# Kernel tuning notes

Hardware: AMD Instinct MI355X
Metric: run time of the kernel (lower is better)

## Reference

```python
import jax, jax.numpy as jnp
import numpy as np

N_NODES = 50000
N_EDGES = 640000
D = 128
L = 3


def setup_inputs() -> dict:
    key = jax.random.key(0)
    k1, k2, k3, k4 = jax.random.split(key, 4)
    x = jax.random.normal(k1, (N_NODES, D), dtype=jnp.float32)
    # Glorot-ish scale so activations stay O(1) across 3 layers
    Ws = jax.random.normal(k2, (L, D, D), dtype=jnp.float32) * (1.0 / np.sqrt(D))
    bs = jnp.zeros((L, D), dtype=jnp.float32)
    edge_src = jax.random.randint(k3, (N_EDGES,), 0, N_NODES, dtype=jnp.int32)
    edge_dst = jax.random.randint(k4, (N_EDGES,), 0, N_NODES, dtype=jnp.int32)
    return {"x": x, "Ws": Ws, "bs": bs, "edge_src": edge_src, "edge_dst": edge_dst}


def reference(x, Ws, bs, edge_src, edge_dst):
    n = x.shape[0]
    ones = jnp.ones(edge_src.shape[0], dtype=x.dtype)
    # degrees, clamped to 1 as in dgl GraphConv(norm='both')
    deg_out = jnp.maximum(jax.ops.segment_sum(ones, edge_src, num_segments=n), 1.0)
    deg_in = jnp.maximum(jax.ops.segment_sum(ones, edge_dst, num_segments=n), 1.0)
    inv_sqrt_out = jax.lax.rsqrt(deg_out)[:, None]  # [N,1]
    inv_sqrt_in = jax.lax.rsqrt(deg_in)[:, None]    # [N,1]
    for l in range(Ws.shape[0]):
        h = x * inv_sqrt_out                         # src normalization
        msg = h[edge_src]                            # [E,D] gather
        agg = jax.ops.segment_sum(msg, edge_dst, num_segments=n)  # [N,D] scatter-add
        h = agg * inv_sqrt_in                        # dst normalization
        x = jax.nn.relu(h @ Ws[l] + bs[l])           # linear + ReLU
    return x
```

## Files before the change

### kernel.cpp

```cpp
#include <hip/hip_runtime.h>
#include <hip/hip_fp16.h>

typedef __attribute__((ext_vector_type(8))) _Float16 half8;
typedef __attribute__((ext_vector_type(4))) float f32x4;
typedef unsigned int u32;
typedef unsigned short u16;
typedef unsigned long long u64;

#define ELL_PAD 64
#define BKT 128
#define BKT_SH 7
#define EPB 2048
#define NAMAX 512
#define RUNCAP 3072


__global__ __launch_bounds__(256) void initpack(int* __restrict__ deg_out,
                                                u32* __restrict__ xz0,
                                                u32* __restrict__ xz1,
                                                const float* __restrict__ Ws,
                                                _Float16* __restrict__ Whi,
                                                _Float16* __restrict__ Wlo,
                                                int N, int padU32, int zb, int packTotal) {
  int b = blockIdx.x;
  if (b < zb) {
    int i = b * 256 + threadIdx.x;
    if (i < N) deg_out[i] = 0;
    if (b == 0) {
      for (int j = threadIdx.x; j < padU32; j += 256) { xz0[j] = 0; xz1[j] = 0; }
    }
    return;
  }
  int i = (b - zb) * 256 + threadIdx.x;
  if (i < packTotal) {
    int lane  = i & 63;
    int kstep = (i >> 6) & 3;
    int ntile = (i >> 8) & 7;
    int layer = i >> 11;
    int nn = ntile * 16 + (lane & 15);
    int k0 = kstep * 32 + (lane >> 4) * 8;
    const float* W = Ws + (size_t)layer * 128 * 128;
    size_t base = (size_t)i * 8;
    for (int j = 0; j < 8; j++) {
      float v = W[(k0 + j) * 128 + nn];
      _Float16 hi = (_Float16)v;
      Whi[base + j] = hi;
      Wlo[base + j] = (_Float16)(v - (float)hi);
    }
  }
}


__global__ __launch_bounds__(512) void parta(const int* __restrict__ esrc,
                                             const int* __restrict__ edst,
                                             int* __restrict__ deg_out,
                                             u32* __restrict__ part,
                                             u32* __restrict__ runTab,
                                             int E, int NB) {
  __shared__ u32 hist[512];
  __shared__ u32 stage[EPB];
  __shared__ u32 scanA[512];
  int a = blockIdx.x;
  int e0 = a * EPB;
  int e1 = min(E, e0 + EPB);
  int len = e1 - e0;
  int tid = threadIdx.x;
  if (tid <= NB) hist[tid] = 0;
  __syncthreads();
  for (int i = e0 + tid; i < e1; i += 512) {
    int s = esrc[i];
    int d = edst[i];
    atomicAdd(&deg_out[s], 1);
    atomicAdd(&hist[d >> BKT_SH], 1u);
  }
  __syncthreads();
  u32 myc = (tid < NB) ? hist[tid] : 0;
  scanA[tid] = myc;
  __syncthreads();
  for (int off = 1; off < NB; off <<= 1) {
    u32 t = scanA[tid] + ((tid >= off) ? scanA[tid - off] : 0);
    __syncthreads();
    scanA[tid] = t;
    __syncthreads();
  }
  u32 excl = scanA[tid] - myc;
  u32* rt = runTab + (size_t)a * (NB + 1);
  if (tid < NB) { rt[tid] = excl; hist[tid] = excl; }
  if (tid == 0) rt[NB] = (u32)len;
  __syncthreads();
  for (int i = e0 + tid; i < e1; i += 512) {
    int s = esrc[i];
    int d = edst[i];
    u32 p = atomicAdd(&hist[d >> BKT_SH], 1u);
    stage[p] = (u32)s | ((u32)(d & (BKT - 1)) << 16);
  }
  __syncthreads();
  u32* op = part + (size_t)a * EPB;
  for (int j = tid; j < len; j += 512) op[j] = stage[j];
}


__global__ __launch_bounds__(512) void partb(const u32* __restrict__ part,
                                             const u32* __restrict__ runTab,
                                             int* __restrict__ deg_in,
                                             u16* __restrict__ ell,
                                             int N, int NA, int NB) {
  __shared__ u16 slice[BKT * ELL_PAD];
  __shared__ u32 cnt2[BKT * 17];
  __shared__ u32 roff[NAMAX + 1];
  __shared__ u32 rbase[NAMAX];
  __shared__ u16 runid[RUNCAP];
  __shared__ u32 pstage[RUNCAP];
  __shared__ u32 scanA[512];
  int b = blockIdx.x;
  int base = b * BKT;
  int hi = min(BKT, N - base);
  if (hi <= 0) return;
  int tid = threadIdx.x;

  u32 nv = ((u32)N << 16) | (u32)N;
  u32* s32 = (u32*)slice;
  for (int j = tid; j < BKT * (ELL_PAD / 2); j += 512) s32[j] = nv;
  for (int j = tid; j < BKT * 17; j += 512) cnt2[j] = 0;
  u32 mylen = 0;
  if (tid < NA) {
    u32 s = runTab[(size_t)tid * (NB + 1) + b];
    u32 e = runTab[(size_t)tid * (NB + 1) + b + 1];
    mylen = e - s;
    rbase[tid] = (u32)tid * EPB + s;
  }
  scanA[tid] = mylen;
  __syncthreads();
  for (int off = 1; off < NA + 1; off <<= 1) {
    u32 t = scanA[tid] + ((tid >= off) ? scanA[tid - off] : 0);
    __syncthreads();
    scanA[tid] = t;
    __syncthreads();
  }
  if (tid <= NA) roff[tid] = scanA[tid] - mylen;
  __syncthreads();
  int T = (int)roff[NA];
  for (int a = tid; a < NA; a += 512) {
    u32 s0 = roff[a];
    u32 l  = roff[a + 1] - s0;
    for (u32 k = 0; k < l; k++)
      if (s0 + k < RUNCAP) runid[s0 + k] = (u16)a;
  }
  __syncthreads();
  for (int i = tid; i < T; i += 512) {
    int a;
    if (i < RUNCAP) a = runid[i];
    else {
      int lo = 0, hh = NA;
      while (hh - lo > 1) { int mid = (lo + hh) >> 1; if (roff[mid] <= (u32)i) lo = mid; else hh = mid; }
      a = lo;
    }
    u32 pair = part[(size_t)rbase[a] + ((u32)i - roff[a])];
    if (i < RUNCAP) pstage[i] = pair;
    u32 dl  = pair >> 16;
    u32 src = pair & 0xFFFFu;
    atomicAdd(&cnt2[dl * 17 + (src >> 12)], 1u);
  }
  __syncthreads();
  if (tid < BKT) {
    u32 run = 0;
    for (int bk = 0; bk < 16; bk++) {
      u32 t = cnt2[tid * 17 + bk];
      cnt2[tid * 17 + bk] = run;
      run += t;
    }
    if (tid < hi) deg_in[base + tid] = (int)run;
  }
  __syncthreads();
  for (int i = tid; i < T; i += 512) {
    u32 pair;
    if (i < RUNCAP) pair = pstage[i];
    else {
      int lo = 0, hh = NA;
      while (hh - lo > 1) { int mid = (lo + hh) >> 1; if (roff[mid] <= (u32)i) lo = mid; else hh = mid; }
      pair = part[(size_t)rbase[lo] + ((u32)i - roff[lo])];
    }
    u32 dl  = pair >> 16;
    u32 src = pair & 0xFFFFu;
    u32 p = atomicAdd(&cnt2[dl * 17 + (src >> 12)], 1u);
    if (p < ELL_PAD) slice[dl * ELL_PAD + p] = (u16)src;
  }
  __syncthreads();
  u32* eg = (u32*)(ell + (size_t)base * ELL_PAD);
  for (int j = tid; j < hi * (ELL_PAD / 2); j += 512) eg[j] = s32[j];
}


__global__ __launch_bounds__(256) void xscale(const float* __restrict__ x,
                                              const int* __restrict__ deg_out,
                                              __half2* __restrict__ xh, int n64) {
  int gid = blockIdx.x * 256 + threadIdx.x;
  if (gid >= n64) return;
  int row = gid >> 6;
  int d = deg_out[row]; if (d < 1) d = 1;
  float s = rsqrtf((float)d);
  float2 v = ((const float2*)x)[gid];
  xh[gid] = __floats2half2_rn(v.x * s, v.y * s);
}


__global__ __launch_bounds__(512) void layer16(const _Float16* __restrict__ xh,
                                               const int* __restrict__ deg_in,
                                               const u16* __restrict__ ell,
                                               const _Float16* __restrict__ Whi,
                                               const _Float16* __restrict__ Wlo,
                                               const float* __restrict__ bias,
                                               const int* __restrict__ deg_out,
                                               __half* __restrict__ out16,
                                               float* __restrict__ out32, int n) {
  __shared__ _Float16 As[16 * 136];
  const int wave = threadIdx.x >> 6;
  const int lane = threadIdx.x & 63;
  const int sub  = lane & 15;
  const int grp  = lane >> 4;
  const int sh   = grp << 4;
  const u32 sub16 = (u32)sub * 16u;
  const int rowBase = blockIdx.x * 16;
  const char* __restrict__ xb = (const char*)xh;

  {
    int r0 = rowBase + wave * 2, r1 = r0 + 1;
    int d0 = (r0 < n) ? deg_in[r0] : 0;
    int d1 = (r1 < n) ? deg_in[r1] : 0;
    int l0 = d0 > ELL_PAD ? ELL_PAD : d0;
    int l1 = d1 > ELL_PAD ? ELL_PAD : d1;
    int t0 = (l0 + 3) & ~3;
    int t1 = (l1 + 3) & ~3;
    const u16* ep0 = ell + (u32)(r0 < n ? r0 : 0) * ELL_PAD;
    const u16* ep1 = ell + (u32)(r1 < n ? r1 : 0) * ELL_PAD;

    float a0[8] = {0.f, 0.f, 0.f, 0.f, 0.f, 0.f, 0.f, 0.f};
    float a1[8] = {0.f, 0.f, 0.f, 0.f, 0.f, 0.f, 0.f, 0.f};

    int m = t0 < t1 ? t0 : t1;
    int e = 0;
    for (; e + 8 <= m; e += 8) {
      u64 wa0 = *(const u64*)&ep0[e];
      u64 wa1 = *(const u64*)&ep0[e + 4];
      u64 wb0 = *(const u64*)&ep1[e];
      u64 wb1 = *(const u64*)&ep1[e + 4];
      u32 ia0 = ((u32)(wa0 >> sh) & 0xFFFFu) * 256u + sub16;
      u32 ia1 = ((u32)(wa1 >> sh) & 0xFFFFu) * 256u + sub16;
      u32 ib0 = ((u32)(wb0 >> sh) & 0xFFFFu) * 256u + sub16;
      u32 ib1 = ((u32)(wb1 >> sh) & 0xFFFFu) * 256u + sub16;
      half8 va0 = *(const half8*)(xb + ia0);
      half8 va1 = *(const half8*)(xb + ia1);
      half8 vb0 = *(const half8*)(xb + ib0);
      half8 vb1 = *(const half8*)(xb + ib1);
#pragma unroll
      for (int j = 0; j < 8; j++) {
        a0[j] += (float)va0[j] + (float)va1[j];
        a1[j] += (float)vb0[j] + (float)vb1[j];
      }
    }
    for (; e < m; e += 4) {
      u64 wa = *(const u64*)&ep0[e];
      u64 wb = *(const u64*)&ep1[e];
      u32 ia = ((u32)(wa >> sh) & 0xFFFFu) * 256u + sub16;
      u32 ib = ((u32)(wb >> sh) & 0xFFFFu) * 256u + sub16;
      half8 va = *(const half8*)(xb + ia);
      half8 vb = *(const half8*)(xb + ib);
#pragma unroll
      for (int j = 0; j < 8; j++) { a0[j] += (float)va[j]; a1[j] += (float)vb[j]; }
    }
    for (int ea = m; ea < t0; ea += 4) {
      u64 wa = *(const u64*)&ep0[ea];
      u32 ia = ((u32)(wa >> sh) & 0xFFFFu) * 256u + sub16;
      half8 va = *(const half8*)(xb + ia);
#pragma unroll
      for (int j = 0; j < 8; j++) a0[j] += (float)va[j];
    }
    for (int eb = m; eb < t1; eb += 4) {
      u64 wb = *(const u64*)&ep1[eb];
      u32 ib = ((u32)(wb >> sh) & 0xFFFFu) * 256u + sub16;
      half8 vb = *(const half8*)(xb + ib);
#pragma unroll
      for (int j = 0; j < 8; j++) a1[j] += (float)vb[j];
    }

#pragma unroll
    for (int j = 0; j < 8; j++) {
      a0[j] += __shfl_xor(a0[j], 16, 64);
      a0[j] += __shfl_xor(a0[j], 32, 64);
      a1[j] += __shfl_xor(a1[j], 16, 64);
      a1[j] += __shfl_xor(a1[j], 32, 64);
    }

    float si0 = rsqrtf((float)(d0 < 1 ? 1 : d0));
    float si1 = rsqrtf((float)(d1 < 1 ? 1 : d1));
    if (grp == 0) {
      half8 h0, h1;
#pragma unroll
      for (int j = 0; j < 8; j++) {
        h0[j] = (_Float16)(a0[j] * si0);
        h1[j] = (_Float16)(a1[j] * si1);
      }
      *(half8*)&As[(wave * 2 + 0) * 136 + sub * 8] = h0;
      *(half8*)&As[(wave * 2 + 1) * 136 + sub * 8] = h1;
    }
  }
  __syncthreads();

  f32x4 acc = (f32x4){0.f, 0.f, 0.f, 0.f};
#pragma unroll
  for (int ks = 0; ks < 4; ks++) {
    half8 a  = *(const half8*)&As[(size_t)sub * 136 + ks * 32 + grp * 8];
    half8 bh = *(const half8*)&Whi[((wave * 4 + ks) * 64 + lane) * 8];
    half8 bl = *(const half8*)&Wlo[((wave * 4 + ks) * 64 + lane) * 8];
    acc = __builtin_amdgcn_mfma_f32_16x16x32_f16(a, bh, acc, 0, 0, 0);
    acc = __builtin_amdgcn_mfma_f32_16x16x32_f16(a, bl, acc, 0, 0, 0);
  }

  const int r0c = rowBase + grp * 4;
  const int col = wave * 16 + sub;
  const float bv = bias[col];
#pragma unroll
  for (int r = 0; r < 4; r++) {
    int row = r0c + r;
    if (row < n) {
      float v = fmaxf(acc[r] + bv, 0.f);
      if (out16) {
        int d = deg_out[row]; if (d < 1) d = 1;
        out16[(size_t)row * 128 + col] = __float2half(v * rsqrtf((float)d));
      } else {
        out32[(size_t)row * 128 + col] = v;
      }
    }
  }
}


extern "C" void kernel_launch(void* const* d_in, const int* in_sizes, int n_in,
                              void* d_out, int out_size, void* d_ws, size_t ws_size,
                              hipStream_t stream) {
  const float* x   = (const float*)d_in[0];
  const float* Ws  = (const float*)d_in[1];
  const float* bs  = (const float*)d_in[2];
  const int* esrc  = (const int*)d_in[3];
  const int* edst  = (const int*)d_in[4];

  const int D = 128;
  const int N = in_sizes[0] / D;
  const int E = in_sizes[3];
  const int L = in_sizes[1] / (D * D);
  const int Npad = ((N + 15) / 16) * 16;
  const int NA = (E + EPB - 1) / EPB;
  const int NB = (N + BKT - 1) / BKT;

  char* base = (char*)d_ws;
  size_t off = 0;
  auto alloc = [&](size_t bytes) {
    char* p = base + off;
    off = (off + bytes + 255) & ~(size_t)255;
    return p;
  };
  int*      deg_out = (int*)alloc((size_t)N * 4);
  int*      deg_in  = (int*)alloc((size_t)N * 4);
  u16*      ell     = (u16*)alloc((size_t)N * ELL_PAD * 2);
  _Float16* Whi     = (_Float16*)alloc((size_t)L * 16384 * 2);
  _Float16* Wlo     = (_Float16*)alloc((size_t)L * 16384 * 2);
  _Float16* xh0     = (_Float16*)alloc((size_t)(Npad + 16) * 128 * 2);
  _Float16* xh1     = (_Float16*)alloc((size_t)(Npad + 16) * 128 * 2);
  u32*      part    = (u32*)alloc((size_t)NA * EPB * 4);
  u32*      runTab  = (u32*)alloc((size_t)NA * (NB + 1) * 4);

  const int zb = (N + 255) / 256;
  const int packTotal = L * 2048;
  const int packB = (packTotal + 255) / 256;
  const int padU32 = 16 * 64;

  initpack<<<dim3(zb + packB), dim3(256), 0, stream>>>(
      deg_out,
      (u32*)(xh0 + (size_t)N * 128), (u32*)(xh1 + (size_t)N * 128),
      Ws, Whi, Wlo, N, padU32, zb, packTotal);
  parta<<<dim3(NA), dim3(512), 0, stream>>>(
      esrc, edst, deg_out, part, runTab, E, NB);
  partb<<<dim3(NB), dim3(512), 0, stream>>>(
      part, runTab, deg_in, ell, N, NA, NB);
  xscale<<<dim3((N * 64 + 255) / 256), dim3(256), 0, stream>>>(
      x, deg_out, (__half2*)xh0, N * 64);

  float* outf = (float*)d_out;
  _Float16* ping[2] = {xh0, xh1};
  const dim3 lgrid(Npad / 16), lblk(512);

  for (int l = 0; l < L; l++) {
    bool last = (l == L - 1);
    layer16<<<lgrid, lblk, 0, stream>>>(
        (const _Float16*)ping[l & 1], deg_in, ell,
        Whi + (size_t)l * 16384, Wlo + (size_t)l * 16384,
        bs + (size_t)l * D, deg_out,
        last ? nullptr : (__half*)ping[(l + 1) & 1],
        last ? outf : nullptr, N);
  }
}
```

Baseline: 241.6 us.

## Fuse all stages into one persistent cooperative kernel with grid syncs

Replaces the sequence of separate kernels (init/pack, two-pass edge partitioning, x scaling, three layer kernels) with a single persistent cooperative kernel. Stages are separated by grid-wide barriers, and blocks loop over work items. The x scaling step is folded into the ELL-build stage, and one union shared-memory buffer is reused across phases. This targets launch overhead and inter-kernel gaps. The costs are that grid size is capped by occupancy, which may lower parallelism in the heavy gather stage, and the large shared-memory footprint may limit blocks per CU.

New measurement: 485.3 us. 2.01x slower.

```diff
diff --git a/kernel.cpp b/kernel.cpp
--- a/kernel.cpp
+++ b/kernel.cpp
@@ -1,5 +1,8 @@
 #include <hip/hip_runtime.h>
 #include <hip/hip_fp16.h>
+#include <hip/hip_cooperative_groups.h>
+
+namespace cg = cooperative_groups;
 
 typedef __attribute__((ext_vector_type(8))) _Float16 half8;
 typedef __attribute__((ext_vector_type(4))) float f32x4;
@@ -15,320 +18,308 @@
 #define RUNCAP 3072
 
 
-__global__ __launch_bounds__(256) void initpack(int* __restrict__ deg_out,
-                                                u32* __restrict__ xz0,
-                                                u32* __restrict__ xz1,
-                                                const float* __restrict__ Ws,
-                                                _Float16* __restrict__ Whi,
-                                                _Float16* __restrict__ Wlo,
-                                                int N, int padU32, int zb, int packTotal) {
-  int b = blockIdx.x;
-  if (b < zb) {
-    int i = b * 256 + threadIdx.x;
-    if (i < N) deg_out[i] = 0;
-    if (b == 0) {
-      for (int j = threadIdx.x; j < padU32; j += 256) { xz0[j] = 0; xz1[j] = 0; }
+struct Par {
+  const float* x; const float* Ws; const float* bs;
+  const int* esrc; const int* edst;
+  int* deg_out; int* deg_in;
+  u16* ell; _Float16* Whi; _Float16* Wlo;
+  _Float16* xh0; _Float16* xh1; float* outf;
+  u32* part; u32* runTab;
+  int N, E, L, NA, NB, tiles, packTotal, padU32;
+};
+
+__global__ __launch_bounds__(512) void fused_all(Par p) {
+  __shared__ __align__(16) char smem[49680];
+  cg::grid_group grid = cg::this_grid();
+  const int tid = threadIdx.x;
+
+  {
+    int gt = blockIdx.x * 512 + tid, gs = gridDim.x * 512;
+    for (int i = gt; i < p.N; i += gs) p.deg_out[i] = 0;
+    u32* xz0 = (u32*)(p.xh0 + (size_t)p.N * 128);
+    u32* xz1 = (u32*)(p.xh1 + (size_t)p.N * 128);
+    for (int j = gt; j < p.padU32; j += gs) { xz0[j] = 0; xz1[j] = 0; }
+    for (int i = gt; i < p.packTotal; i += gs) {
+      int lane = i & 63, kstep = (i >> 6) & 3, ntile = (i >> 8) & 7, layer = i >> 11;
+      int nn = ntile * 16 + (lane & 15);
+      int k0 = kstep * 32 + (lane >> 4) * 8;
+      const float* W = p.Ws + (size_t)layer * 128 * 128;
+      size_t base = (size_t)i * 8;
+      for (int j = 0; j < 8; j++) {
+        float v = W[(k0 + j) * 128 + nn];
+        _Float16 hi = (_Float16)v;
+        p.Whi[base + j] = hi;
+        p.Wlo[base + j] = (_Float16)(v - (float)hi);
+      }
     }
-    return;
-  }
-  int i = (b - zb) * 256 + threadIdx.x;
-  if (i < packTotal) {
-    int lane  = i & 63;
-    int kstep = (i >> 6) & 3;
-    int ntile = (i >> 8) & 7;
-    int layer = i >> 11;
-    int nn = ntile * 16 + (lane & 15);
-    int k0 = kstep * 32 + (lane >> 4) * 8;
-    const float* W = Ws + (size_t)layer * 128 * 128;
-    size_t base = (size_t)i * 8;
-    for (int j = 0; j < 8; j++) {
-      float v = W[(k0 + j) * 128 + nn];
-      _Float16 hi = (_Float16)v;
-      Whi[base + j] = hi;
-      Wlo[base + j] = (_Float16)(v - (float)hi);
+  }
+  grid.sync();
+
+  {
+    u32* hist  = (u32*)smem;
+    u32* stage = (u32*)(smem + 2048);
+    u32* scanA = (u32*)(smem + 10240);
+    for (int a = blockIdx.x; a < p.NA; a += gridDim.x) {
+      __syncthreads();
+      int e0 = a * EPB, e1 = min(p.E, e0 + EPB), len = e1 - e0;
+      if (tid <= p.NB) hist[tid] = 0;
+      __syncthreads();
+      for (int i = e0 + tid; i < e1; i += 512) {
+        int s = p.esrc[i], d = p.edst[i];
+        atomicAdd(&p.deg_out[s], 1);
+        atomicAdd(&hist[d >> BKT_SH], 1u);
+      }
+      __syncthreads();
+      u32 myc = (tid < p.NB) ? hist[tid] : 0;
+      scanA[tid] = myc;
+      __syncthreads();
+      for (int off = 1; off < p.NB; off <<= 1) {
+        u32 t2 = scanA[tid] + ((tid >= off) ? scanA[tid - off] : 0);
+        __syncthreads();
+        scanA[tid] = t2;
+        __syncthreads();
+      }
+      u32 excl = scanA[tid] - myc;
+      u32* rt = p.runTab + (size_t)a * (p.NB + 1);
+      if (tid < p.NB) { rt[tid] = excl; hist[tid] = excl; }
+      if (tid == 0) rt[p.NB] = (u32)len;
+      __syncthreads();
+      for (int i = e0 + tid; i < e1; i += 512) {
+        int s = p.esrc[i], d = p.edst[i];
+        u32 q = atomicAdd(&hist[d >> BKT_SH], 1u);
+        stage[q] = (u32)s | ((u32)(d & (BKT - 1)) << 16);
+      }
+      __syncthreads();
+      u32* op = p.part + (size_t)a * EPB;
+      for (int j = tid; j < len; j += 512) op[j] = stage[j];
     }
   }
-}
-
-
-__global__ __launch_bounds__(512) void parta(const int* __restrict__ esrc,
-                                             const int* __restrict__ edst,
-                                             int* __restrict__ deg_out,
-                                             u32* __restrict__ part,
-                                             u32* __restrict__ runTab,
-                                             int E, int NB) {
-  __shared__ u32 hist[512];
-  __shared__ u32 stage[EPB];
-  __shared__ u32 scanA[512];
-  int a = blockIdx.x;
-  int e0 = a * EPB;
-  int e1 = min(E, e0 + EPB);
-  int len = e1 - e0;
-  int tid = threadIdx.x;
-  if (tid <= NB) hist[tid] = 0;
-  __syncthreads();
-  for (int i = e0 + tid; i < e1; i += 512) {
-    int s = esrc[i];
-    int d = edst[i];
-    atomicAdd(&deg_out[s], 1);
-    atomicAdd(&hist[d >> BKT_SH], 1u);
-  }
-  __syncthreads();
-  u32 myc = (tid < NB) ? hist[tid] : 0;
-  scanA[tid] = myc;
-  __syncthreads();
-  for (int off = 1; off < NB; off <<= 1) {
-    u32 t = scanA[tid] + ((tid >= off) ? scanA[tid - off] : 0);
-    __syncthreads();
-    scanA[tid] = t;
-    __syncthreads();
-  }
-  u32 excl = scanA[tid] - myc;
-  u32* rt = runTab + (size_t)a * (NB + 1);
-  if (tid < NB) { rt[tid] = excl; hist[tid] = excl; }
-  if (tid == 0) rt[NB] = (u32)len;
-  __syncthreads();
-  for (int i = e0 + tid; i < e1; i += 512) {
-    int s = esrc[i];
-    int d = edst[i];
-    u32 p = atomicAdd(&hist[d >> BKT_SH], 1u);
-    stage[p] = (u32)s | ((u32)(d & (BKT - 1)) << 16);
-  }
-  __syncthreads();
-  u32* op = part + (size_t)a * EPB;
-  for (int j = tid; j < len; j += 512) op[j] = stage[j];
-}
-
-
-__global__ __launch_bounds__(512) void partb(const u32* __restrict__ part,
-                                             const u32* __restrict__ runTab,
-                                             int* __restrict__ deg_in,
-                                             u16* __restrict__ ell,
-                                             int N, int NA, int NB) {
-  __shared__ u16 slice[BKT * ELL_PAD];
-  __shared__ u32 cnt2[BKT * 17];
-  __shared__ u32 roff[NAMAX + 1];
-  __shared__ u32 rbase[NAMAX];
-  __shared__ u16 runid[RUNCAP];
-  __shared__ u32 pstage[RUNCAP];
-  __shared__ u32 scanA[512];
-  int b = blockIdx.x;
-  int base = b * BKT;
-  int hi = min(BKT, N - base);
-  if (hi <= 0) return;
-  int tid = threadIdx.x;
-
-  u32 nv = ((u32)N << 16) | (u32)N;
-  u32* s32 = (u32*)slice;
-  for (int j = tid; j < BKT * (ELL_PAD / 2); j += 512) s32[j] = nv;
-  for (int j = tid; j < BKT * 17; j += 512) cnt2[j] = 0;
-  u32 mylen = 0;
-  if (tid < NA) {
-    u32 s = runTab[(size_t)tid * (NB + 1) + b];
-    u32 e = runTab[(size_t)tid * (NB + 1) + b + 1];
-    mylen = e - s;
-    rbase[tid] = (u32)tid * EPB + s;
-  }
-  scanA[tid] = mylen;
-  __syncthreads();
-  for (int off = 1; off < NA + 1; off <<= 1) {
-    u32 t = scanA[tid] + ((tid >= off) ? scanA[tid - off] : 0);
-    __syncthreads();
-    scanA[tid] = t;
-    __syncthreads();
-  }
-  if (tid <= NA) roff[tid] = scanA[tid] - mylen;
-  __syncthreads();
-  int T = (int)roff[NA];
-  for (int a = tid; a < NA; a += 512) {
-    u32 s0 = roff[a];
-    u32 l  = roff[a + 1] - s0;
-    for (u32 k = 0; k < l; k++)
-      if (s0 + k < RUNCAP) runid[s0 + k] = (u16)a;
-  }
-  __syncthreads();
-  for (int i = tid; i < T; i += 512) {
-    int a;
-    if (i < RUNCAP) a = runid[i];
-    else {
-      int lo = 0, hh = NA;
-      while (hh - lo > 1) { int mid = (lo + hh) >> 1; if (roff[mid] <= (u32)i) lo = mid; else hh = mid; }
-      a = lo;
+  grid.sync();
+
+  {
+    u16* slice  = (u16*)smem;
+    u32* cnt2   = (u32*)(smem + 16384);
+    u32* roff   = (u32*)(smem + 25088);
+    u32* rbase  = (u32*)(smem + 27140);
+    u16* runid  = (u16*)(smem + 29188);
+    u32* pstage = (u32*)(smem + 35332);
+    u32* scanB  = (u32*)(smem + 47620);
+    for (int b = blockIdx.x; b < p.NB; b += gridDim.x) {
+      __syncthreads();
+      int base = b * BKT;
+      int hi = min(BKT, p.N - base);
+      if (hi <= 0) continue;
+      u32 nv = ((u32)p.N << 16) | (u32)p.N;
+      u32* s32 = (u32*)slice;
+      for (int j = tid; j < BKT * (ELL_PAD / 2); j += 512) s32[j] = nv;
+      for (int j = tid; j < BKT * 17; j += 512) cnt2[j] = 0;
+      u32 mylen = 0;
+      if (tid < p.NA) {
+        u32 s = p.runTab[(size_t)tid * (p.NB + 1) + b];
+        u32 e = p.runTab[(size_t)tid * (p.NB + 1) + b + 1];
+        mylen = e - s;
+        rbase[tid] = (u32)tid * EPB + s;
+      }
+      scanB[tid] = mylen;
+      __syncthreads();
+      for (int off = 1; off < p.NA + 1; off <<= 1) {
+        u32 t2 = scanB[tid] + ((tid >= off) ? scanB[tid - off] : 0);
+        __syncthreads();
+        scanB[tid] = t2;
+        __syncthreads();
+      }
+      if (tid <= p.NA) roff[tid] = scanB[tid] - mylen;
+      __syncthreads();
+      int T = (int)roff[p.NA];
+      for (int a = tid; a < p.NA; a += 512) {
+        u32 s0 = roff[a];
+        u32 l = roff[a + 1] - s0;
+        for (u32 k = 0; k < l; k++)
+          if (s0 + k < RUNCAP) runid[s0 + k] = (u16)a;
+      }
+      __syncthreads();
+      for (int i = tid; i < T; i += 512) {
+        int a;
+        if (i < RUNCAP) a = runid[i];
+        else {
+          int lo = 0, hh = p.NA;
+          while (hh - lo > 1) { int mid = (lo + hh) >> 1; if (roff[mid] <= (u32)i) lo = mid; else hh = mid; }
+          a = lo;
+        }
+        u32 pair = p.part[(size_t)rbase[a] + ((u32)i - roff[a])];
+        if (i < RUNCAP) pstage[i] = pair;
+        u32 dl = pair >> 16;
+        u32 src = pair & 0xFFFFu;
+        atomicAdd(&cnt2[dl * 17 + (src >> 12)], 1u);
+      }
+      __syncthreads();
+      if (tid < BKT) {
+        u32 run = 0;
+        for (int bk = 0; bk < 16; bk++) {
+          u32 t2 = cnt2[tid * 17 + bk];
+          cnt2[tid * 17 + bk] = run;
+          run += t2;
+        }
+        if (tid < hi) p.deg_in[base + tid] = (int)run;
+      }
+      __syncthreads();
+      for (int i = tid; i < T; i += 512) {
+        u32 pair;
+        if (i < RUNCAP) pair = pstage[i];
+        else {
+          int lo = 0, hh = p.NA;
+          while (hh - lo > 1) { int mid = (lo + hh) >> 1; if (roff[mid] <= (u32)i) lo = mid; else hh = mid; }
+          pair = p.part[(size_t)rbase[lo] + ((u32)i - roff[lo])];
+        }
+        u32 dl = pair >> 16;
+        u32 src = pair & 0xFFFFu;
+        u32 q = atomicAdd(&cnt2[dl * 17 + (src >> 12)], 1u);
+        if (q < ELL_PAD) slice[dl * ELL_PAD + q] = (u16)src;
+      }
+      __syncthreads();
+      u32* eg = (u32*)(p.ell + (size_t)base * ELL_PAD);
+      for (int j = tid; j < hi * (ELL_PAD / 2); j += 512) eg[j] = s32[j];
+      float* sc = (float*)scanB;
+      if (tid < hi) {
+        int d = p.deg_out[base + tid]; if (d < 1) d = 1;
+        sc[tid] = rsqrtf((float)d);
+      }
+      __syncthreads();
+      __half2* xh2 = (__half2*)p.xh0;
+      for (int j = tid; j < hi * 64; j += 512) {
+        int r = j >> 6, c = j & 63;
+        float s = sc[r];
+        float2 v = ((const float2*)p.x)[(size_t)(base + r) * 64 + c];
+        xh2[(size_t)(base + r) * 64 + c] = __floats2half2_rn(v.x * s, v.y * s);
+      }
     }
-    u32 pair = part[(size_t)rbase[a] + ((u32)i - roff[a])];
-    if (i < RUNCAP) pstage[i] = pair;
-    u32 dl  = pair >> 16;
-    u32 src = pair & 0xFFFFu;
-    atomicAdd(&cnt2[dl * 17 + (src >> 12)], 1u);
-  }
-  __syncthreads();
-  if (tid < BKT) {
-    u32 run = 0;
-    for (int bk = 0; bk < 16; bk++) {
-      u32 t = cnt2[tid * 17 + bk];
-      cnt2[tid * 17 + bk] = run;
-      run += t;
-    }
-    if (tid < hi) deg_in[base + tid] = (int)run;
-  }
-  __syncthreads();
-  for (int i = tid; i < T; i += 512) {
-    u32 pair;
-    if (i < RUNCAP) pair = pstage[i];
-    else {
-      int lo = 0, hh = NA;
-      while (hh - lo > 1) { int mid = (lo + hh) >> 1; if (roff[mid] <= (u32)i) lo = mid; else hh = mid; }
-      pair = part[(size_t)rbase[lo] + ((u32)i - roff[lo])];
-    }
-    u32 dl  = pair >> 16;
-    u32 src = pair & 0xFFFFu;
-    u32 p = atomicAdd(&cnt2[dl * 17 + (src >> 12)], 1u);
-    if (p < ELL_PAD) slice[dl * ELL_PAD + p] = (u16)src;
-  }
-  __syncthreads();
-  u32* eg = (u32*)(ell + (size_t)base * ELL_PAD);
-  for (int j = tid; j < hi * (ELL_PAD / 2); j += 512) eg[j] = s32[j];
-}
-
-
-__global__ __launch_bounds__(256) void xscale(const float* __restrict__ x,
-                                              const int* __restrict__ deg_out,
-                                              __half2* __restrict__ xh, int n64) {
-  int gid = blockIdx.x * 256 + threadIdx.x;
-  if (gid >= n64) return;
-  int row = gid >> 6;
-  int d = deg_out[row]; if (d < 1) d = 1;
-  float s = rsqrtf((float)d);
-  float2 v = ((const float2*)x)[gid];
-  xh[gid] = __floats2half2_rn(v.x * s, v.y * s);
-}
-
-
-__global__ __launch_bounds__(512) void layer16(const _Float16* __restrict__ xh,
-                                               const int* __restrict__ deg_in,
-                                               const u16* __restrict__ ell,
-                                               const _Float16* __restrict__ Whi,
-                                               const _Float16* __restrict__ Wlo,
-                                               const float* __restrict__ bias,
-                                               const int* __restrict__ deg_out,
-                                               __half* __restrict__ out16,
-                                               float* __restrict__ out32, int n) {
-  __shared__ _Float16 As[16 * 136];
-  const int wave = threadIdx.x >> 6;
-  const int lane = threadIdx.x & 63;
-  const int sub  = lane & 15;
-  const int grp  = lane >> 4;
-  const int sh   = grp << 4;
-  const u32 sub16 = (u32)sub * 16u;
-  const int rowBase = blockIdx.x * 16;
-  const char* __restrict__ xb = (const char*)xh;
-
-  {
-    int r0 = rowBase + wave * 2, r1 = r0 + 1;
-    int d0 = (r0 < n) ? deg_in[r0] : 0;
-    int d1 = (r1 < n) ? deg_in[r1] : 0;
-    int l0 = d0 > ELL_PAD ? ELL_PAD : d0;
-    int l1 = d1 > ELL_PAD ? ELL_PAD : d1;
-    int t0 = (l0 + 3) & ~3;
-    int t1 = (l1 + 3) & ~3;
-    const u16* ep0 = ell + (u32)(r0 < n ? r0 : 0) * ELL_PAD;
-    const u16* ep1 = ell + (u32)(r1 < n ? r1 : 0) * ELL_PAD;
-
-    float a0[8] = {0.f, 0.f, 0.f, 0.f, 0.f, 0.f, 0.f, 0.f};
-    float a1[8] = {0.f, 0.f, 0.f, 0.f, 0.f, 0.f, 0.f, 0.f};
-
-    int m = t0 < t1 ? t0 : t1;
-    int e = 0;
-    for (; e + 8 <= m; e += 8) {
-      u64 wa0 = *(const u64*)&ep0[e];
-      u64 wa1 = *(const u64*)&ep0[e + 4];
-      u64 wb0 = *(const u64*)&ep1[e];
-      u64 wb1 = *(const u64*)&ep1[e + 4];
-      u32 ia0 = ((u32)(wa0 >> sh) & 0xFFFFu) * 256u + sub16;
-      u32 ia1 = ((u32)(wa1 >> sh) & 0xFFFFu) * 256u + sub16;
-      u32 ib0 = ((u32)(wb0 >> sh) & 0xFFFFu) * 256u + sub16;
-      u32 ib1 = ((u32)(wb1 >> sh) & 0xFFFFu) * 256u + sub16;
-      half8 va0 = *(const half8*)(xb + ia0);
-      half8 va1 = *(const half8*)(xb + ia1);
-      half8 vb0 = *(const half8*)(xb + ib0);
-      half8 vb1 = *(const half8*)(xb + ib1);
-#pragma unroll
-      for (int j = 0; j < 8; j++) {
-        a0[j] += (float)va0[j] + (float)va1[j];
-        a1[j] += (float)vb0[j] + (float)vb1[j];
-      }
-    }
-    for (; e < m; e += 4) {
-      u64 wa = *(const u64*)&ep0[e];
-      u64 wb = *(const u64*)&ep1[e];
-      u32 ia = ((u32)(wa >> sh) & 0xFFFFu) * 256u + sub16;
-      u32 ib = ((u32)(wb >> sh) & 0xFFFFu) * 256u + sub16;
-      half8 va = *(const half8*)(xb + ia);
-      half8 vb = *(const half8*)(xb + ib);
-#pragma unroll
-      for (int j = 0; j < 8; j++) { a0[j] += (float)va[j]; a1[j] += (float)vb[j]; }
-    }
-    for (int ea = m; ea < t0; ea += 4) {
-      u64 wa = *(const u64*)&ep0[ea];
-      u32 ia = ((u32)(wa >> sh) & 0xFFFFu) * 256u + sub16;
-      half8 va = *(const half8*)(xb + ia);
-#pragma unroll
-      for (int j = 0; j < 8; j++) a0[j] += (float)va[j];
-    }
-    for (int eb = m; eb < t1; eb += 4) {
-      u64 wb = *(const u64*)&ep1[eb];
-      u32 ib = ((u32)(wb >> sh) & 0xFFFFu) * 256u + sub16;
-      half8 vb = *(const half8*)(xb + ib);
-#pragma unroll
-      for (int j = 0; j < 8; j++) a1[j] += (float)vb[j];
-    }
-
-#pragma unroll
-    for (int j = 0; j < 8; j++) {
-      a0[j] += __shfl_xor(a0[j], 16, 64);
-      a0[j] += __shfl_xor(a0[j], 32, 64);
-      a1[j] += __shfl_xor(a1[j], 16, 64);
-      a1[j] += __shfl_xor(a1[j], 32, 64);
-    }
-
-    float si0 = rsqrtf((float)(d0 < 1 ? 1 : d0));
-    float si1 = rsqrtf((float)(d1 < 1 ? 1 : d1));
-    if (grp == 0) {
-      half8 h0, h1;
-#pragma unroll
-      for (int j = 0; j < 8; j++) {
-        h0[j] = (_Float16)(a0[j] * si0);
-        h1[j] = (_Float16)(a1[j] * si1);
-      }
-      *(half8*)&As[(wave * 2 + 0) * 136 + sub * 8] = h0;
-      *(half8*)&As[(wave * 2 + 1) * 136 + sub * 8] = h1;
-    }
-  }
-  __syncthreads();
-
-  f32x4 acc = (f32x4){0.f, 0.f, 0.f, 0.f};
-#pragma unroll
-  for (int ks = 0; ks < 4; ks++) {
-    half8 a  = *(const half8*)&As[(size_t)sub * 136 + ks * 32 + grp * 8];
-    half8 bh = *(const half8*)&Whi[((wave * 4 + ks) * 64 + lane) * 8];
-    half8 bl = *(const half8*)&Wlo[((wave * 4 + ks) * 64 + lane) * 8];
-    acc = __builtin_amdgcn_mfma_f32_16x16x32_f16(a, bh, acc, 0, 0, 0);
-    acc = __builtin_amdgcn_mfma_f32_16x16x32_f16(a, bl, acc, 0, 0, 0);
-  }
-
-  const int r0c = rowBase + grp * 4;
-  const int col = wave * 16 + sub;
-  const float bv = bias[col];
-#pragma unroll
-  for (int r = 0; r < 4; r++) {
-    int row = r0c + r;
-    if (row < n) {
-      float v = fmaxf(acc[r] + bv, 0.f);
-      if (out16) {
-        int d = deg_out[row]; if (d < 1) d = 1;
-        out16[(size_t)row * 128 + col] = __float2half(v * rsqrtf((float)d));
-      } else {
-        out32[(size_t)row * 128 + col] = v;
+  }
+
+  for (int l = 0; l < p.L; l++) {
+    grid.sync();
+    const _Float16* xin = (l & 1) ? p.xh1 : p.xh0;
+    bool last = (l == p.L - 1);
+    __half* o16 = last ? nullptr : (__half*)((l & 1) ? p.xh0 : p.xh1);
+    float* o32 = last ? p.outf : nullptr;
+    const _Float16* Wh = p.Whi + (size_t)l * 16384;
+    const _Float16* Wl = p.Wlo + (size_t)l * 16384;
+    const float* bias = p.bs + (size_t)l * 128;
+    _Float16* As = (_Float16*)smem;
+    const int wave = tid >> 6, lane = tid & 63, sub = lane & 15, grp = lane >> 4;
+    const int sh = grp << 4;
+    const u32 sub16 = (u32)sub * 16u;
+    const char* xb = (const char*)xin;
+
+    for (int t = blockIdx.x; t < p.tiles; t += gridDim.x) {
+      __syncthreads();
+      int rowBase = t * 16;
+      {
+        int r0 = rowBase + wave * 2, r1 = r0 + 1;
+        int d0 = (r0 < p.N) ? p.deg_in[r0] : 0;
+        int d1 = (r1 < p.N) ? p.deg_in[r1] : 0;
+        int l0 = d0 > ELL_PAD ? ELL_PAD : d0;
+        int l1 = d1 > ELL_PAD ? ELL_PAD : d1;
+        int t0 = (l0 + 3) & ~3;
+        int t1 = (l1 + 3) & ~3;
+        const u16* ep0 = p.ell + (u32)(r0 < p.N ? r0 : 0) * ELL_PAD;
+        const u16* ep1 = p.ell + (u32)(r1 < p.N ? r1 : 0) * ELL_PAD;
+
+        float a0[8] = {0.f, 0.f, 0.f, 0.f, 0.f, 0.f, 0.f, 0.f};
+        float a1[8] = {0.f, 0.f, 0.f, 0.f, 0.f, 0.f, 0.f, 0.f};
+
+        int m = t0 < t1 ? t0 : t1;
+        int e = 0;
+        for (; e + 8 <= m; e += 8) {
+          u64 wa0 = *(const u64*)&ep0[e];
+          u64 wa1 = *(const u64*)&ep0[e + 4];
+          u64 wb0 = *(const u64*)&ep1[e];
+          u64 wb1 = *(const u64*)&ep1[e + 4];
+          u32 ia0 = ((u32)(wa0 >> sh) & 0xFFFFu) * 256u + sub16;
+          u32 ia1 = ((u32)(wa1 >> sh) & 0xFFFFu) * 256u + sub16;
+          u32 ib0 = ((u32)(wb0 >> sh) & 0xFFFFu) * 256u + sub16;
+          u32 ib1 = ((u32)(wb1 >> sh) & 0xFFFFu) * 256u + sub16;
+          half8 va0 = *(const half8*)(xb + ia0);
+          half8 va1 = *(const half8*)(xb + ia1);
+          half8 vb0 = *(const half8*)(xb + ib0);
+          half8 vb1 = *(const half8*)(xb + ib1);
+#pragma unroll
+          for (int j = 0; j < 8; j++) {
+            a0[j] += (float)va0[j] + (float)va1[j];
+            a1[j] += (float)vb0[j] + (float)vb1[j];
+          }
+        }
+        for (; e < m; e += 4) {
+          u64 wa = *(const u64*)&ep0[e];
+          u64 wb = *(const u64*)&ep1[e];
+          u32 ia = ((u32)(wa >> sh) & 0xFFFFu) * 256u + sub16;
+          u32 ib = ((u32)(wb >> sh) & 0xFFFFu) * 256u + sub16;
+          half8 va = *(const half8*)(xb + ia);
+          half8 vb = *(const half8*)(xb + ib);
+#pragma unroll
+          for (int j = 0; j < 8; j++) { a0[j] += (float)va[j]; a1[j] += (float)vb[j]; }
+        }
+        for (int ea = m; ea < t0; ea += 4) {
+          u64 wa = *(const u64*)&ep0[ea];
+          u32 ia = ((u32)(wa >> sh) & 0xFFFFu) * 256u + sub16;
+          half8 va = *(const half8*)(xb + ia);
+#pragma unroll
+          for (int j = 0; j < 8; j++) a0[j] += (float)va[j];
+        }
+        for (int eb = m; eb < t1; eb += 4) {
+          u64 wb = *(const u64*)&ep1[eb];
+          u32 ib = ((u32)(wb >> sh) & 0xFFFFu) * 256u + sub16;
+          half8 vb = *(const half8*)(xb + ib);
+#pragma unroll
+          for (int j = 0; j < 8; j++) a1[j] += (float)vb[j];
+        }
+
+#pragma unroll
+        for (int j = 0; j < 8; j++) {
+          a0[j] += __shfl_xor(a0[j], 16, 64);
+          a0[j] += __shfl_xor(a0[j], 32, 64);
+          a1[j] += __shfl_xor(a1[j], 16, 64);
+          a1[j] += __shfl_xor(a1[j], 32, 64);
+        }
+
+        float si0 = rsqrtf((float)(d0 < 1 ? 1 : d0));
+        float si1 = rsqrtf((float)(d1 < 1 ? 1 : d1));
+        if (grp == 0) {
+          half8 h0, h1;
+#pragma unroll
+          for (int j = 0; j < 8; j++) {
+            h0[j] = (_Float16)(a0[j] * si0);
+            h1[j] = (_Float16)(a1[j] * si1);
+          }
+          *(half8*)&As[(wave * 2 + 0) * 136 + sub * 8] = h0;
+          *(half8*)&As[(wave * 2 + 1) * 136 + sub * 8] = h1;
+        }
+      }
+      __syncthreads();
+
+      f32x4 acc = (f32x4){0.f, 0.f, 0.f, 0.f};
+#pragma unroll
+      for (int ks = 0; ks < 4; ks++) {
+        half8 a = *(const half8*)&As[(size_t)sub * 136 + ks * 32 + grp * 8];
+        half8 bh = *(const half8*)&Wh[((wave * 4 + ks) * 64 + lane) * 8];
+        half8 bl = *(const half8*)&Wl[((wave * 4 + ks) * 64 + lane) * 8];
+        acc = __builtin_amdgcn_mfma_f32_16x16x32_f16(a, bh, acc, 0, 0, 0);
+        acc = __builtin_amdgcn_mfma_f32_16x16x32_f16(a, bl, acc, 0, 0, 0);
+      }
+      const int r0c = rowBase + grp * 4;
+      const int col = wave * 16 + sub;
+      const float bv = bias[col];
+#pragma unroll
+      for (int r = 0; r < 4; r++) {
+        int row = r0c + r;
+        if (row < p.N) {
+          float v = fmaxf(acc[r] + bv, 0.f);
+          if (o16) {
+            int d = p.deg_out[row]; if (d < 1) d = 1;
+            o16[(size_t)row * 128 + col] = __float2half(v * rsqrtf((float)d));
+          } else {
+            o32[(size_t)row * 128 + col] = v;
+          }
+        }
       }
     }
   }
@@ -369,33 +360,26 @@
   u32*      part    = (u32*)alloc((size_t)NA * EPB * 4);
   u32*      runTab  = (u32*)alloc((size_t)NA * (NB + 1) * 4);
 
-  const int zb = (N + 255) / 256;
-  const int packTotal = L * 2048;
-  const int packB = (packTotal + 255) / 256;
-  const int padU32 = 16 * 64;
-
-  initpack<<<dim3(zb + packB), dim3(256), 0, stream>>>(
-      deg_out,
-      (u32*)(xh0 + (size_t)N * 128), (u32*)(xh1 + (size_t)N * 128),
-      Ws, Whi, Wlo, N, padU32, zb, packTotal);
-  parta<<<dim3(NA), dim3(512), 0, stream>>>(
-      esrc, edst, deg_out, part, runTab, E, NB);
-  partb<<<dim3(NB), dim3(512), 0, stream>>>(
-      part, runTab, deg_in, ell, N, NA, NB);
-  xscale<<<dim3((N * 64 + 255) / 256), dim3(256), 0, stream>>>(
-      x, deg_out, (__half2*)xh0, N * 64);
-
-  float* outf = (float*)d_out;
-  _Float16* ping[2] = {xh0, xh1};
-  const dim3 lgrid(Npad / 16), lblk(512);
-
-  for (int l = 0; l < L; l++) {
-    bool last = (l == L - 1);
-    layer16<<<lgrid, lblk, 0, stream>>>(
-        (const _Float16*)ping[l & 1], deg_in, ell,
-        Whi + (size_t)l * 16384, Wlo + (size_t)l * 16384,
-        bs + (size_t)l * D, deg_out,
-        last ? nullptr : (__half*)ping[(l + 1) & 1],
-        last ? outf : nullptr, N);
-  }
+  static int coopGrid = 0;
+  if (coopGrid == 0) {
+    int bpc = 0, dev = 0, cus = 0;
+    hipGetDevice(&dev);
+    hipDeviceGetAttribute(&cus, hipDeviceAttributeMultiprocessorCount, dev);
+    hipOccupancyMaxActiveBlocksPerMultiprocessor(&bpc, fused_all, 512, 0);
+    if (bpc < 1) bpc = 1;
+    if (cus < 1) cus = 256;
+    coopGrid = bpc * cus;
+  }
+
+  Par par;
+  par.x = x; par.Ws = Ws; par.bs = bs; par.esrc = esrc; par.edst = edst;
+  par.deg_out = deg_out; par.deg_in = deg_in; par.ell = ell;
+  par.Whi = Whi; par.Wlo = Wlo; par.xh0 = xh0; par.xh1 = xh1;
+  par.outf = (float*)d_out; par.part = part; par.runTab = runTab;
+  par.N = N; par.E = E; par.L = L; par.NA = NA; par.NB = NB;
+  par.tiles = Npad / 16; par.packTotal = L * 2048; par.padU32 = 16 * 64;
+
+  void* args[] = { &par };
+  hipLaunchCooperativeKernel((const void*)fused_all, dim3(coopGrid), dim3(512),
+                             args, 0, stream);
 }
```

## Halve partition bucket sizes and fuse source-scaling pass into partb

Applied to the files above, without the earlier changes.

Bucket width drops from 128 to 64 nodes and edges per partition block from 2048 to 1024. That doubles the block count in both partition kernels, so each block has less serial work and shared memory. Both prefix scans now have each thread handle two elements so they still fit 512 threads. The separate xscale kernel is removed; each partb block writes the deg_out-scaled fp16 copy of x for its own node range, saving one launch. The trade-off is that partb does more per block and every block reads a larger run table.

Result: no change. 241.8 us (+0.1%).

```diff
diff --git a/kernel.cpp b/kernel.cpp
--- a/kernel.cpp
+++ b/kernel.cpp
@@ -8,11 +8,11 @@
 typedef unsigned long long u64;
 
 #define ELL_PAD 64
-#define BKT 128
-#define BKT_SH 7
-#define EPB 2048
-#define NAMAX 512
-#define RUNCAP 3072
+#define BKT 64
+#define BKT_SH 6
+#define EPB 1024
+#define NAMAX 640
+#define RUNCAP 1536
 
 
 __global__ __launch_bounds__(256) void initpack(int* __restrict__ deg_out,
@@ -57,7 +57,7 @@
                                              u32* __restrict__ part,
                                              u32* __restrict__ runTab,
                                              int E, int NB) {
-  __shared__ u32 hist[512];
+  __shared__ u32 hist[1024];
   __shared__ u32 stage[EPB];
   __shared__ u32 scanA[512];
   int a = blockIdx.x;
@@ -65,7 +65,7 @@
   int e1 = min(E, e0 + EPB);
   int len = e1 - e0;
   int tid = threadIdx.x;
-  if (tid <= NB) hist[tid] = 0;
+  for (int j = tid; j <= NB; j += 512) hist[j] = 0;
   __syncthreads();
   for (int i = e0 + tid; i < e1; i += 512) {
     int s = esrc[i];
@@ -74,18 +74,22 @@
     atomicAdd(&hist[d >> BKT_SH], 1u);
   }
   __syncthreads();
-  u32 myc = (tid < NB) ? hist[tid] : 0;
-  scanA[tid] = myc;
-  __syncthreads();
-  for (int off = 1; off < NB; off <<= 1) {
-    u32 t = scanA[tid] + ((tid >= off) ? scanA[tid - off] : 0);
+  int i0 = 2 * tid, i1 = 2 * tid + 1;
+  u32 c0 = (i0 < NB) ? hist[i0] : 0;
+  u32 c1 = (i1 < NB) ? hist[i1] : 0;
+  u32 s2 = c0 + c1;
+  scanA[tid] = s2;
+  __syncthreads();
+  for (int off = 1; off < 512; off <<= 1) {
+    u32 t2 = scanA[tid] + ((tid >= off) ? scanA[tid - off] : 0);
     __syncthreads();
-    scanA[tid] = t;
+    scanA[tid] = t2;
     __syncthreads();
   }
-  u32 excl = scanA[tid] - myc;
+  u32 base = scanA[tid] - s2;
   u32* rt = runTab + (size_t)a * (NB + 1);
-  if (tid < NB) { rt[tid] = excl; hist[tid] = excl; }
+  if (i0 < NB) { rt[i0] = base;      hist[i0] = base; }
+  if (i1 < NB) { rt[i1] = base + c0; hist[i1] = base + c0; }
   if (tid == 0) rt[NB] = (u32)len;
   __syncthreads();
   for (int i = e0 + tid; i < e1; i += 512) {
@@ -102,8 +106,11 @@
 
 __global__ __launch_bounds__(512) void partb(const u32* __restrict__ part,
                                              const u32* __restrict__ runTab,
+                                             const float* __restrict__ x,
+                                             const int* __restrict__ deg_out,
                                              int* __restrict__ deg_in,
                                              u16* __restrict__ ell,
+                                             __half2* __restrict__ xh,
                                              int N, int NA, int NB) {
   __shared__ u16 slice[BKT * ELL_PAD];
   __shared__ u32 cnt2[BKT * 17];
@@ -111,7 +118,7 @@
   __shared__ u32 rbase[NAMAX];
   __shared__ u16 runid[RUNCAP];
   __shared__ u32 pstage[RUNCAP];
-  __shared__ u32 scanA[512];
+  __shared__ u32 scanB[512];
   int b = blockIdx.x;
   int base = b * BKT;
   int hi = min(BKT, N - base);
@@ -122,27 +129,38 @@
   u32* s32 = (u32*)slice;
   for (int j = tid; j < BKT * (ELL_PAD / 2); j += 512) s32[j] = nv;
   for (int j = tid; j < BKT * 17; j += 512) cnt2[j] = 0;
-  u32 mylen = 0;
-  if (tid < NA) {
-    u32 s = runTab[(size_t)tid * (NB + 1) + b];
-    u32 e = runTab[(size_t)tid * (NB + 1) + b + 1];
-    mylen = e - s;
-    rbase[tid] = (u32)tid * EPB + s;
-  }
-  scanA[tid] = mylen;
-  __syncthreads();
-  for (int off = 1; off < NA + 1; off <<= 1) {
-    u32 t = scanA[tid] + ((tid >= off) ? scanA[tid - off] : 0);
+  int a0 = 2 * tid, a1 = 2 * tid + 1;
+  u32 l0 = 0, l1 = 0;
+  if (a0 < NA) {
+    u32 s = runTab[(size_t)a0 * (NB + 1) + b];
+    u32 e = runTab[(size_t)a0 * (NB + 1) + b + 1];
+    l0 = e - s;
+    rbase[a0] = (u32)a0 * EPB + s;
+  }
+  if (a1 < NA) {
+    u32 s = runTab[(size_t)a1 * (NB + 1) + b];
+    u32 e = runTab[(size_t)a1 * (NB + 1) + b + 1];
+    l1 = e - s;
+    rbase[a1] = (u32)a1 * EPB + s;
+  }
+  u32 s2 = l0 + l1;
+  scanB[tid] = s2;
+  __syncthreads();
+  for (int off = 1; off < 512; off <<= 1) {
+    u32 t2 = scanB[tid] + ((tid >= off) ? scanB[tid - off] : 0);
     __syncthreads();
-    scanA[tid] = t;
+    scanB[tid] = t2;
     __syncthreads();
   }
-  if (tid <= NA) roff[tid] = scanA[tid] - mylen;
+  u32 pbase = scanB[tid] - s2;
+  if (a0 < NA) roff[a0] = pbase;
+  if (a1 < NA) roff[a1] = pbase + l0;
+  if (tid == 511) roff[NA] = scanB[511];
   __syncthreads();
   int T = (int)roff[NA];
   for (int a = tid; a < NA; a += 512) {
     u32 s0 = roff[a];
-    u32 l  = roff[a + 1] - s0;
+    u32 l = roff[a + 1] - s0;
     for (u32 k = 0; k < l; k++)
       if (s0 + k < RUNCAP) runid[s0 + k] = (u16)a;
   }
@@ -157,7 +175,7 @@
     }
     u32 pair = part[(size_t)rbase[a] + ((u32)i - roff[a])];
     if (i < RUNCAP) pstage[i] = pair;
-    u32 dl  = pair >> 16;
+    u32 dl = pair >> 16;
     u32 src = pair & 0xFFFFu;
     atomicAdd(&cnt2[dl * 17 + (src >> 12)], 1u);
   }
@@ -165,9 +183,9 @@
   if (tid < BKT) {
     u32 run = 0;
     for (int bk = 0; bk < 16; bk++) {
-      u32 t = cnt2[tid * 17 + bk];
+      u32 t2 = cnt2[tid * 17 + bk];
       cnt2[tid * 17 + bk] = run;
-      run += t;
+      run += t2;
     }
     if (tid < hi) deg_in[base + tid] = (int)run;
   }
@@ -180,7 +198,7 @@
       while (hh - lo > 1) { int mid = (lo + hh) >> 1; if (roff[mid] <= (u32)i) lo = mid; else hh = mid; }
       pair = part[(size_t)rbase[lo] + ((u32)i - roff[lo])];
     }
-    u32 dl  = pair >> 16;
+    u32 dl = pair >> 16;
     u32 src = pair & 0xFFFFu;
     u32 p = atomicAdd(&cnt2[dl * 17 + (src >> 12)], 1u);
     if (p < ELL_PAD) slice[dl * ELL_PAD + p] = (u16)src;
@@ -188,19 +206,18 @@
   __syncthreads();
   u32* eg = (u32*)(ell + (size_t)base * ELL_PAD);
   for (int j = tid; j < hi * (ELL_PAD / 2); j += 512) eg[j] = s32[j];
-}
-
-
-__global__ __launch_bounds__(256) void xscale(const float* __restrict__ x,
-                                              const int* __restrict__ deg_out,
-                                              __half2* __restrict__ xh, int n64) {
-  int gid = blockIdx.x * 256 + threadIdx.x;
-  if (gid >= n64) return;
-  int row = gid >> 6;
-  int d = deg_out[row]; if (d < 1) d = 1;
-  float s = rsqrtf((float)d);
-  float2 v = ((const float2*)x)[gid];
-  xh[gid] = __floats2half2_rn(v.x * s, v.y * s);
+  float* sc = (float*)scanB;
+  if (tid < hi) {
+    int d = deg_out[base + tid]; if (d < 1) d = 1;
+    sc[tid] = rsqrtf((float)d);
+  }
+  __syncthreads();
+  for (int j = tid; j < hi * 64; j += 512) {
+    int r = j >> 6, c = j & 63;
+    float s = sc[r];
+    float2 v = ((const float2*)x)[(size_t)(base + r) * 64 + c];
+    xh[(size_t)(base + r) * 64 + c] = __floats2half2_rn(v.x * s, v.y * s);
+  }
 }
 
 
@@ -381,9 +398,7 @@
   parta<<<dim3(NA), dim3(512), 0, stream>>>(
       esrc, edst, deg_out, part, runTab, E, NB);
   partb<<<dim3(NB), dim3(512), 0, stream>>>(
-      part, runTab, deg_in, ell, N, NA, NB);
-  xscale<<<dim3((N * 64 + 255) / 256), dim3(256), 0, stream>>>(
-      x, deg_out, (__half2*)xh0, N * 64);
+      part, runTab, x, deg_out, deg_in, ell, (__half2*)xh0, N, NA, NB);
 
   float* outf = (float*)d_out;
   _Float16* ping[2] = {xh0, xh1};
```
